# Kernel tuning notes

Hardware: AMD Instinct MI355X
Metric: run time of the kernel (lower is better)

Reference implementation:

```python
import jax, jax.numpy as jnp
import numpy as np

LEVEL = 3
FILT_LEN = 2  # haar
INV_SQRT2 = 0.7071067811865476


def _get_pad(n, flen=FILT_LEN):
    # matches _get_pad in the torch source: returns (pad_right/bottom, pad_left/top)
    p = (2 * flen - 3) // 2
    return p + (n % 2), p


def _dwt_kernel(dec_lo, dec_hi, c):
    # construct_2d_filt: outer products, stacked [ll, lh, hl, hh]
    lo = dec_lo.reshape(-1)
    hi = dec_hi.reshape(-1)
    ll = jnp.outer(lo, lo)
    lh = jnp.outer(hi, lo)
    hl = jnp.outer(lo, hi)
    hh = jnp.outer(hi, hi)
    filt = jnp.stack([ll, lh, hl, hh], 0)        # [4, 2, 2]
    # repeat(c,1,1).unsqueeze(1) -> depthwise kernel [4c, 1, 2, 2]
    return jnp.tile(filt, (c, 1, 1))[:, None]


def setup_inputs():
    key = jax.random.key(0)
    x = jax.random.normal(key, (16, 64, 256, 256), dtype=jnp.float32)
    # haar filter bank, flipped (flip=True in get_filter_tensors):
    # dec_lo = [s, s] (palindrome), dec_hi flipped = [s, -s]
    dec_lo = jnp.array([[INV_SQRT2, INV_SQRT2]], dtype=jnp.float32)
    dec_hi = jnp.array([[INV_SQRT2, -INV_SQRT2]], dtype=jnp.float32)
    return {"x": x, "dec_lo": dec_lo, "dec_hi": dec_hi}


def reference(x, dec_lo, dec_hi):
    b, c, _, _ = x.shape
    kernel = _dwt_kernel(dec_lo, dec_hi, c)      # [4c, 1, 2, 2]
    details = []
    l = x
    for _ in range(LEVEL):
        padb, padt = _get_pad(l.shape[-2])
        padr, padl = _get_pad(l.shape[-1])
        lp = jnp.pad(l, ((0, 0), (0, 0), (padt, padb), (padl, padr)), mode="edge")
        h = jax.lax.conv_general_dilated(
            lp, kernel, window_strides=(2, 2), padding="VALID",
            feature_group_count=c,
            dimension_numbers=("NCHW", "OIHW", "NCHW"))
        hh_, ww_ = h.shape[-2], h.shape[-1]
        res = h.reshape(b, c, 4, hh_, ww_)       # rearrange 'b (c f) h w -> b c f h w'
        l = res[:, :, 0]
        details.append((res[:, :, 1], res[:, :, 2], res[:, :, 3]))
    # wavelet_component[::-1]: coarsest approximation first, then details coarse->fine
    return (l, *details[::-1])
```

## Files before the change

### kernel.cpp

```cpp
#include <hip/hip_runtime.h>


#define S3       1048576
#define S2       4194304
#define S1       16777216

typedef float v4f __attribute__((ext_vector_type(4)));
typedef float v2f __attribute__((ext_vector_type(2)));

__device__ __forceinline__ v4f ntload4(const float* p) {
    return __builtin_nontemporal_load((const v4f*)p);
}
__device__ __forceinline__ void ntstore4(float* p, v4f v) {
    __builtin_nontemporal_store(v, (v4f*)p);
}
__device__ __forceinline__ void ntstore2(float* p, v2f v) {
    __builtin_nontemporal_store(v, (v2f*)p);
}
__device__ __forceinline__ void ntstore1(float* p, float v) {
    __builtin_nontemporal_store(v, p);
}

__global__ __launch_bounds__(256) void dwt3_haar(const float* __restrict__ x,
                                                 float* __restrict__ out) {
    const int bid = blockIdx.x;
    const int p   = bid >> 2;
    const int s   = bid & 3;
    const int tid = threadIdx.x;
    const int tx  = tid & 31;
    const int ty  = tid >> 5;

    const float* in = x + (size_t)p * 65536
                        + (size_t)(64 * s + 8 * ty) * 256
                        + (size_t)(8 * tx);

    float* __restrict__ l3  = out;
    float* __restrict__ lh3 = out + (size_t)S3;
    float* __restrict__ hl3 = out + (size_t)2 * S3;
    float* __restrict__ hh3 = out + (size_t)3 * S3;
    float* __restrict__ lh2 = out + (size_t)4 * S3;
    float* __restrict__ hl2 = out + (size_t)4 * S3 + S2;
    float* __restrict__ hh2 = out + (size_t)4 * S3 + 2 * (size_t)S2;
    float* __restrict__ lh1 = out + (size_t)4 * S3 + 3 * (size_t)S2;
    float* __restrict__ hl1 = out + (size_t)4 * S3 + 3 * (size_t)S2 + (size_t)S1;
    float* __restrict__ hh1 = out + (size_t)4 * S3 + 3 * (size_t)S2 + 2 * (size_t)S1;

    v4f ra[8], rb[8];
#pragma unroll
    for (int i = 0; i < 8; ++i) {
        ra[i] = ntload4(in + (size_t)i * 256);
        rb[i] = ntload4(in + (size_t)i * 256 + 4);
    }

    float ll1[4][4];

#pragma unroll
    for (int rp = 0; rp < 4; ++rp) {
        const float r0[8] = {ra[2*rp].x, ra[2*rp].y, ra[2*rp].z, ra[2*rp].w,
                             rb[2*rp].x, rb[2*rp].y, rb[2*rp].z, rb[2*rp].w};
        const float r1[8] = {ra[2*rp+1].x, ra[2*rp+1].y, ra[2*rp+1].z, ra[2*rp+1].w,
                             rb[2*rp+1].x, rb[2*rp+1].y, rb[2*rp+1].z, rb[2*rp+1].w};

        float lhv[4], hlv[4], hhv[4];
#pragma unroll
        for (int j = 0; j < 4; ++j) {
            const float a = r0[2 * j], b = r0[2 * j + 1];
            const float c = r1[2 * j], d = r1[2 * j + 1];
            const float s1 = a + b, s2 = c + d;
            const float d1 = a - b, d2 = c - d;
            ll1[rp][j] = 0.5f * (s1 + s2);
            lhv[j]     = 0.5f * (s1 - s2);
            hlv[j]     = 0.5f * (d1 + d2);
            hhv[j]     = 0.5f * (d1 - d2);
        }
        const size_t o1 = (size_t)p * 16384
                        + (size_t)(32 * s + 4 * ty + rp) * 128
                        + (size_t)(4 * tx);
        ntstore4(lh1 + o1, (v4f){lhv[0], lhv[1], lhv[2], lhv[3]});
        ntstore4(hl1 + o1, (v4f){hlv[0], hlv[1], hlv[2], hlv[3]});
        ntstore4(hh1 + o1, (v4f){hhv[0], hhv[1], hhv[2], hhv[3]});
    }

    float ll2[2][2];
#pragma unroll
    for (int rp = 0; rp < 2; ++rp) {
        float lhv[2], hlv[2], hhv[2];
#pragma unroll
        for (int j = 0; j < 2; ++j) {
            const float a = ll1[2 * rp][2 * j],     b = ll1[2 * rp][2 * j + 1];
            const float c = ll1[2 * rp + 1][2 * j], d = ll1[2 * rp + 1][2 * j + 1];
            const float s1 = a + b, s2 = c + d;
            const float d1 = a - b, d2 = c - d;
            ll2[rp][j] = 0.5f * (s1 + s2);
            lhv[j]     = 0.5f * (s1 - s2);
            hlv[j]     = 0.5f * (d1 + d2);
            hhv[j]     = 0.5f * (d1 - d2);
        }
        const size_t o2 = (size_t)p * 4096
                        + (size_t)(16 * s + 2 * ty + rp) * 64
                        + (size_t)(2 * tx);
        ntstore2(lh2 + o2, (v2f){lhv[0], lhv[1]});
        ntstore2(hl2 + o2, (v2f){hlv[0], hlv[1]});
        ntstore2(hh2 + o2, (v2f){hhv[0], hhv[1]});
    }

    {
        const float a = ll2[0][0], b = ll2[0][1];
        const float c = ll2[1][0], d = ll2[1][1];
        const float s1 = a + b, s2 = c + d;
        const float d1 = a - b, d2 = c - d;
        const size_t o3 = (size_t)p * 1024
                        + (size_t)(8 * s + ty) * 32
                        + (size_t)tx;
        ntstore1(l3  + o3, 0.5f * (s1 + s2));
        ntstore1(lh3 + o3, 0.5f * (s1 - s2));
        ntstore1(hl3 + o3, 0.5f * (d1 + d2));
        ntstore1(hh3 + o3, 0.5f * (d1 - d2));
    }
}

extern "C" void kernel_launch(void* const* d_in, const int* in_sizes, int n_in,
                              void* d_out, int out_size, void* d_ws, size_t ws_size,
                              hipStream_t stream) {
    const float* x = (const float*)d_in[0];
    float* out = (float*)d_out;
    dwt3_haar<<<4096, 256, 0, stream>>>(x, out);
}
```

Before: 433.3 us.

## Remap threads to 4-wide by 16-row tiles with shuffle for level 3

Result: no change. 425.3 us (-1.8%).

```diff
diff --git a/kernel.cpp b/kernel.cpp
--- a/kernel.cpp
+++ b/kernel.cpp
@@ -11,9 +11,6 @@
 __device__ __forceinline__ v4f ntload4(const float* p) {
     return __builtin_nontemporal_load((const v4f*)p);
 }
-__device__ __forceinline__ void ntstore4(float* p, v4f v) {
-    __builtin_nontemporal_store(v, (v4f*)p);
-}
 __device__ __forceinline__ void ntstore2(float* p, v2f v) {
     __builtin_nontemporal_store(v, (v2f*)p);
 }
@@ -21,18 +18,18 @@
     __builtin_nontemporal_store(v, p);
 }
 
-__global__ __launch_bounds__(256) void dwt3_haar(const float* __restrict__ x,
-                                                 float* __restrict__ out) {
+__global__ __launch_bounds__(256) void dwt3_haar_r4(const float* __restrict__ x,
+                                                    float* __restrict__ out) {
     const int bid = blockIdx.x;
     const int p   = bid >> 2;
     const int s   = bid & 3;
     const int tid = threadIdx.x;
-    const int tx  = tid & 31;
-    const int ty  = tid >> 5;
+    const int l   = tid & 63;
+    const int w   = tid >> 6;
 
     const float* in = x + (size_t)p * 65536
-                        + (size_t)(64 * s + 8 * ty) * 256
-                        + (size_t)(8 * tx);
+                        + (size_t)(64 * s + 16 * w) * 256
+                        + (size_t)(4 * l);
 
     float* __restrict__ l3  = out;
     float* __restrict__ lh3 = out + (size_t)S3;
@@ -45,27 +42,21 @@
     float* __restrict__ hl1 = out + (size_t)4 * S3 + 3 * (size_t)S2 + (size_t)S1;
     float* __restrict__ hh1 = out + (size_t)4 * S3 + 3 * (size_t)S2 + 2 * (size_t)S1;
 
-    v4f ra[8], rb[8];
+    v4f row[16];
 #pragma unroll
-    for (int i = 0; i < 8; ++i) {
-        ra[i] = ntload4(in + (size_t)i * 256);
-        rb[i] = ntload4(in + (size_t)i * 256 + 4);
-    }
+    for (int r = 0; r < 16; ++r)
+        row[r] = ntload4(in + (size_t)r * 256);
 
-    float ll1[4][4];
-
+    float ll1[8][2];
 #pragma unroll
-    for (int rp = 0; rp < 4; ++rp) {
-        const float r0[8] = {ra[2*rp].x, ra[2*rp].y, ra[2*rp].z, ra[2*rp].w,
-                             rb[2*rp].x, rb[2*rp].y, rb[2*rp].z, rb[2*rp].w};
-        const float r1[8] = {ra[2*rp+1].x, ra[2*rp+1].y, ra[2*rp+1].z, ra[2*rp+1].w,
-                             rb[2*rp+1].x, rb[2*rp+1].y, rb[2*rp+1].z, rb[2*rp+1].w};
-
-        float lhv[4], hlv[4], hhv[4];
+    for (int rp = 0; rp < 8; ++rp) {
+        const v4f t = row[2 * rp];
+        const v4f u = row[2 * rp + 1];
+        float lhv[2], hlv[2], hhv[2];
 #pragma unroll
-        for (int j = 0; j < 4; ++j) {
-            const float a = r0[2 * j], b = r0[2 * j + 1];
-            const float c = r1[2 * j], d = r1[2 * j + 1];
+        for (int j = 0; j < 2; ++j) {
+            const float a = t[2 * j], b = t[2 * j + 1];
+            const float c = u[2 * j], d = u[2 * j + 1];
             const float s1 = a + b, s2 = c + d;
             const float d1 = a - b, d2 = c - d;
             ll1[rp][j] = 0.5f * (s1 + s2);
@@ -74,48 +65,46 @@
             hhv[j]     = 0.5f * (d1 - d2);
         }
         const size_t o1 = (size_t)p * 16384
-                        + (size_t)(32 * s + 4 * ty + rp) * 128
-                        + (size_t)(4 * tx);
-        ntstore4(lh1 + o1, (v4f){lhv[0], lhv[1], lhv[2], lhv[3]});
-        ntstore4(hl1 + o1, (v4f){hlv[0], hlv[1], hlv[2], hlv[3]});
-        ntstore4(hh1 + o1, (v4f){hhv[0], hhv[1], hhv[2], hhv[3]});
+                        + (size_t)(32 * s + 8 * w + rp) * 128
+                        + (size_t)(2 * l);
+        ntstore2(lh1 + o1, (v2f){lhv[0], lhv[1]});
+        ntstore2(hl1 + o1, (v2f){hlv[0], hlv[1]});
+        ntstore2(hh1 + o1, (v2f){hhv[0], hhv[1]});
     }
 
-    float ll2[2][2];
+    float ll2[4];
 #pragma unroll
-    for (int rp = 0; rp < 2; ++rp) {
-        float lhv[2], hlv[2], hhv[2];
-#pragma unroll
-        for (int j = 0; j < 2; ++j) {
-            const float a = ll1[2 * rp][2 * j],     b = ll1[2 * rp][2 * j + 1];
-            const float c = ll1[2 * rp + 1][2 * j], d = ll1[2 * rp + 1][2 * j + 1];
-            const float s1 = a + b, s2 = c + d;
-            const float d1 = a - b, d2 = c - d;
-            ll2[rp][j] = 0.5f * (s1 + s2);
-            lhv[j]     = 0.5f * (s1 - s2);
-            hlv[j]     = 0.5f * (d1 + d2);
-            hhv[j]     = 0.5f * (d1 - d2);
-        }
+    for (int rp = 0; rp < 4; ++rp) {
+        const float a = ll1[2 * rp][0],     b = ll1[2 * rp][1];
+        const float c = ll1[2 * rp + 1][0], d = ll1[2 * rp + 1][1];
+        const float s1 = a + b, s2 = c + d;
+        const float d1 = a - b, d2 = c - d;
+        ll2[rp] = 0.5f * (s1 + s2);
         const size_t o2 = (size_t)p * 4096
-                        + (size_t)(16 * s + 2 * ty + rp) * 64
-                        + (size_t)(2 * tx);
-        ntstore2(lh2 + o2, (v2f){lhv[0], lhv[1]});
-        ntstore2(hl2 + o2, (v2f){hlv[0], hlv[1]});
-        ntstore2(hh2 + o2, (v2f){hhv[0], hhv[1]});
+                        + (size_t)(16 * s + 4 * w + rp) * 64
+                        + (size_t)l;
+        ntstore1(lh2 + o2, 0.5f * (s1 - s2));
+        ntstore1(hl2 + o2, 0.5f * (d1 + d2));
+        ntstore1(hh2 + o2, 0.5f * (d1 - d2));
     }
 
-    {
-        const float a = ll2[0][0], b = ll2[0][1];
-        const float c = ll2[1][0], d = ll2[1][1];
-        const float s1 = a + b, s2 = c + d;
-        const float d1 = a - b, d2 = c - d;
-        const size_t o3 = (size_t)p * 1024
-                        + (size_t)(8 * s + ty) * 32
-                        + (size_t)tx;
-        ntstore1(l3  + o3, 0.5f * (s1 + s2));
-        ntstore1(lh3 + o3, 0.5f * (s1 - s2));
-        ntstore1(hl3 + o3, 0.5f * (d1 + d2));
-        ntstore1(hh3 + o3, 0.5f * (d1 - d2));
+#pragma unroll
+    for (int q = 0; q < 2; ++q) {
+        const float own0 = ll2[2 * q];
+        const float own1 = ll2[2 * q + 1];
+        const float par0 = __shfl_xor(own0, 1);
+        const float par1 = __shfl_xor(own1, 1);
+        const float s1 = own0 + par0, s2 = own1 + par1;
+        const float d1 = own0 - par0, d2 = own1 - par1;
+        if ((l & 1) == 0) {
+            const size_t o3 = (size_t)p * 1024
+                            + (size_t)(8 * s + 2 * w + q) * 32
+                            + (size_t)(l >> 1);
+            ntstore1(l3  + o3, 0.5f * (s1 + s2));
+            ntstore1(lh3 + o3, 0.5f * (s1 - s2));
+            ntstore1(hl3 + o3, 0.5f * (d1 + d2));
+            ntstore1(hh3 + o3, 0.5f * (d1 - d2));
+        }
     }
 }
 
@@ -124,5 +113,5 @@
                               hipStream_t stream) {
     const float* x = (const float*)d_in[0];
     float* out = (float*)d_out;
-    dwt3_haar<<<4096, 256, 0, stream>>>(x, out);
+    dwt3_haar_r4<<<4096, 256, 0, stream>>>(x, out);
 }
```
